# Performance work log

Measured on AMD Instinct MI355X. Metric: run time of the kernel, lower is better.

The kernel has to match this reference:

```python
import jax, jax.numpy as jnp
import numpy as np

N_NODES = 50000
N_GRAPHS = 64
NEG_SLOPE = 0.2


def gat_conv(x, src, dst, W, a_src, a_dst, b, n_nodes, concat):
    """PyG-style GATConv (eval mode, self-loops already in src/dst).
    x: [N, Fin], W: [Fin, H*C], a_src/a_dst: [H, C], b: [H*C] or [C].
    """
    H, C = a_src.shape
    h = (x @ W).reshape(n_nodes, H, C)                      # [N,H,C]
    al_src = jnp.einsum('nhc,hc->nh', h, a_src)             # [N,H]
    al_dst = jnp.einsum('nhc,hc->nh', h, a_dst)             # [N,H]
    e = jax.nn.leaky_relu(al_src[src] + al_dst[dst], NEG_SLOPE)  # [E,H]
    # softmax over incoming edges per destination node
    m = jax.ops.segment_max(e, dst, num_segments=n_nodes)   # [N,H]
    ex = jnp.exp(e - m[dst])
    s = jax.ops.segment_sum(ex, dst, num_segments=n_nodes)  # [N,H]
    alpha = ex / (s[dst] + 1e-16)                           # [E,H]
    # attention-weighted aggregation of source features
    out = jax.ops.segment_sum(h[src] * alpha[..., None], dst, num_segments=n_nodes)  # [N,H,C]
    out = out.reshape(n_nodes, H * C) if concat else out.mean(axis=1)
    return out + b


def setup_inputs() -> dict:
    key = jax.random.key(0)
    ks = jax.random.split(key, 12)
    n, e = N_NODES, 800000
    x = jax.random.normal(ks[0], (n, 500), dtype=jnp.float32)
    edge_index = jax.random.randint(ks[1], (2, e), 0, n, dtype=jnp.int64)
    batch = jnp.sort(jax.random.randint(ks[2], (n,), 0, N_GRAPHS, dtype=jnp.int64))
    hid, heads = 64, 4
    sc = 0.1
    W1 = jax.random.normal(ks[3], (500, heads * hid), dtype=jnp.float32) * sc
    a_src1 = jax.random.normal(ks[4], (heads, hid), dtype=jnp.float32) * sc
    a_dst1 = jax.random.normal(ks[5], (heads, hid), dtype=jnp.float32) * sc
    b1 = jnp.zeros((heads * hid,), dtype=jnp.float32)
    W2 = jax.random.normal(ks[6], (heads * hid, hid), dtype=jnp.float32) * sc
    a_src2 = jax.random.normal(ks[7], (1, hid), dtype=jnp.float32) * sc
    a_dst2 = jax.random.normal(ks[8], (1, hid), dtype=jnp.float32) * sc
    b2 = jnp.zeros((hid,), dtype=jnp.float32)
    Wl = jax.random.normal(ks[9], (hid, 2), dtype=jnp.float32) * sc
    bl = jnp.zeros((2,), dtype=jnp.float32)
    return dict(x=x, edge_index=edge_index, batch=batch,
                W1=W1, a_src1=a_src1, a_dst1=a_dst1, b1=b1,
                W2=W2, a_src2=a_src2, a_dst2=a_dst2, b2=b2,
                Wl=Wl, bl=bl)


def reference(x, edge_index, batch, W1, a_src1, a_dst1, b1,
              W2, a_src2, a_dst2, b2, Wl, bl):
    n = x.shape[0]
    # PyG GATConv adds self-loops by default
    loops = jnp.arange(n, dtype=edge_index.dtype)
    src = jnp.concatenate([edge_index[0], loops])
    dst = jnp.concatenate([edge_index[1], loops])
    h = jax.nn.relu(gat_conv(x, src, dst, W1, a_src1, a_dst1, b1, n, concat=True))
    h = jax.nn.relu(gat_conv(h, src, dst, W2, a_src2, a_dst2, b2, n, concat=False))
    # global mean pool over graphs
    sums = jax.ops.segment_sum(h, batch, num_segments=N_GRAPHS)      # [G, hid]
    cnt = jax.ops.segment_sum(jnp.ones((n,), h.dtype), batch, num_segments=N_GRAPHS)
    pooled = sums / jnp.maximum(cnt, 1.0)[:, None]
    return pooled @ Wl + bl                                          # [G, 2]
```

## Files before the change

kernel.cpp:

```cpp
#include <hip/hip_runtime.h>
#include <math.h>

#define NN   50000
#define NE   800000
#define NET  850000
#define NG   64
#define KIN  500
#define NEG  0.2f

typedef unsigned short ushort_t;
typedef __attribute__((ext_vector_type(8))) short bf8_t;
typedef __attribute__((ext_vector_type(8))) unsigned short us8_t;
typedef __attribute__((ext_vector_type(4))) float f4_t;

__device__ __forceinline__ float bf2f(ushort_t u) {
    unsigned v = ((unsigned)u) << 16;
    return __builtin_bit_cast(float, v);
}
__device__ __forceinline__ ushort_t f2bf(float f) {
    unsigned b = __builtin_bit_cast(unsigned, f);
    unsigned r = (b + 0x7FFFu + ((b >> 16) & 1u)) >> 16;
    return (ushort_t)r;
}

#define GLOAD_LDS(g, l)                                                        \
    __builtin_amdgcn_global_load_lds(                                          \
        (const __attribute__((address_space(1))) unsigned int*)(g),            \
        (__attribute__((address_space(3))) unsigned int*)(l), 16, 0, 0)

__global__ void k_deg(const int* __restrict__ ei, int* __restrict__ deg) {
    int e = blockIdx.x * 256 + threadIdx.x;
    if (e >= NET) return;
    int dst = (e < NE) ? ei[NE + e] : (e - NE);
    atomicAdd(&deg[dst], 1);
}

__global__ void k_scan_part(const int* __restrict__ deg, int* __restrict__ part) {
    __shared__ int s[256];
    int t = threadIdx.x;
    int i = blockIdx.x * 256 + t;
    s[t] = (i < NN) ? deg[i] : 0;
    __syncthreads();
    for (int off = 128; off > 0; off >>= 1) {
        if (t < off) s[t] += s[t + off];
        __syncthreads();
    }
    if (t == 0) part[blockIdx.x] = s[0];
}

__global__ void k_scan_top(int* __restrict__ part, int nb) {
    __shared__ int s[256];
    int t = threadIdx.x;
    int v = (t < nb) ? part[t] : 0;
    s[t] = v;
    __syncthreads();
    for (int off = 1; off < 256; off <<= 1) {
        int a = (t >= off) ? s[t - off] : 0;
        __syncthreads();
        s[t] += a;
        __syncthreads();
    }
    if (t < nb) part[t] = s[t] - v;
}

__global__ void k_scan_apply(const int* __restrict__ deg, const int* __restrict__ part,
                             int* __restrict__ rowptr) {
    __shared__ int s[256];
    int t = threadIdx.x;
    int i = blockIdx.x * 256 + t;
    int v = (i < NN) ? deg[i] : 0;
    s[t] = v;
    __syncthreads();
    for (int off = 1; off < 256; off <<= 1) {
        int a = (t >= off) ? s[t - off] : 0;
        __syncthreads();
        s[t] += a;
        __syncthreads();
    }
    if (i < NN) rowptr[i] = part[blockIdx.x] + s[t] - v;
    if (i == 0) rowptr[NN] = NET;
}

__global__ void k_fill(const int* __restrict__ ei, const int* __restrict__ rowptr,
                       int* __restrict__ cursor, int* __restrict__ csr) {
    int e = blockIdx.x * 256 + threadIdx.x;
    if (e >= NET) return;
    int src, dst;
    if (e < NE) { src = ei[e]; dst = ei[NE + e]; }
    else        { src = dst = e - NE; }
    int pos = atomicAdd(&cursor[dst], 1);
    csr[rowptr[dst] + pos] = src;
}

__global__ void k_cast_x(const float* __restrict__ x, ushort_t* __restrict__ xb) {
    int idx = blockIdx.x * 256 + threadIdx.x;
    if (idx >= 50048 * 128) return;
    int row = idx >> 7, k4 = (idx & 127) * 4;
    ushort4 o = make_ushort4(0, 0, 0, 0);
    if (row < NN && k4 < KIN) {
        float4 v = *(const float4*)&x[(size_t)row * KIN + k4];
        o.x = f2bf(v.x); o.y = f2bf(v.y); o.z = f2bf(v.z); o.w = f2bf(v.w);
    }
    *(ushort4*)&xb[(size_t)idx * 4] = o;
}

template <int KSRC, int KPAD, int NOUT>
__global__ void k_cast_wt(const float* __restrict__ W, ushort_t* __restrict__ Wt) {
    int idx = blockIdx.x * 256 + threadIdx.x;
    if (idx >= NOUT * KPAD) return;
    int n = idx / KPAD, k = idx - n * KPAD;
    float v = (k < KSRC) ? W[(size_t)k * NOUT + n] : 0.f;
    Wt[idx] = f2bf(v);
}

template <int K, int LDA, int BM, int BN, int WM, int FOUT, int HEADS>
__global__ __launch_bounds__(256) void k_mfma(
    const ushort_t* __restrict__ A, const ushort_t* __restrict__ Wt,
    const float* __restrict__ a_s, const float* __restrict__ a_d,
    ushort_t* __restrict__ Hb, float* __restrict__ als, float* __restrict__ ald)
{
    __shared__ __align__(16) ushort_t lA[BM * 32];
    __shared__ __align__(16) ushort_t lB[BN * 32];
    const int t    = threadIdx.x;
    const int row0 = blockIdx.y * BM;
    const int n0   = blockIdx.x * BN;
    const int ww   = t >> 6, lane = t & 63;
    const int wm   = ww % WM, wn = ww / WM;
    const int lrow = lane & 15, lq = lane >> 4;

    f4_t acc[4][4] = {};

    for (int k0 = 0; k0 < K; k0 += 32) {
#pragma unroll
        for (int i = 0; i < BM / 64; i++) {
            int c = i * 256 + t;
            int row = c >> 2, kq = c & 3;
            const ushort_t* gp = A + (size_t)(row0 + row) * LDA + k0 + kq * 8;
            GLOAD_LDS(gp, &lA[c * 8]);
        }
#pragma unroll
        for (int i = 0; i < BN / 64; i++) {
            int c = i * 256 + t;
            int row = c >> 2, kq = c & 3;
            const ushort_t* gp = Wt + (size_t)(n0 + row) * K + k0 + kq * 8;
            GLOAD_LDS(gp, &lB[c * 8]);
        }
        __syncthreads();
        bf8_t af[4], bfr[4];
#pragma unroll
        for (int i = 0; i < 4; i++)
            af[i] = *(const bf8_t*)&lA[(wm * 64 + i * 16 + lrow) * 32 + lq * 8];
#pragma unroll
        for (int j = 0; j < 4; j++)
            bfr[j] = *(const bf8_t*)&lB[(wn * 64 + j * 16 + lrow) * 32 + lq * 8];
#pragma unroll
        for (int i = 0; i < 4; i++)
#pragma unroll
            for (int j = 0; j < 4; j++)
                acc[i][j] = __builtin_amdgcn_mfma_f32_16x16x32_bf16(af[i], bfr[j], acc[i][j], 0, 0, 0);
        __syncthreads();
    }

    const int head = (n0 + wn * 64) >> 6;
    float as4[4], ad4[4];
#pragma unroll
    for (int j = 0; j < 4; j++) {
        as4[j] = a_s[head * 64 + j * 16 + lrow];
        ad4[j] = a_d[head * 64 + j * 16 + lrow];
    }
#pragma unroll
    for (int i = 0; i < 4; i++) {
#pragma unroll
        for (int r = 0; r < 4; r++) {
            int row = row0 + wm * 64 + i * 16 + lq * 4 + r;
            float v0 = acc[i][0][r], v1 = acc[i][1][r], v2 = acc[i][2][r], v3 = acc[i][3][r];
            if (row < NN) {
                size_t base = (size_t)row * FOUT + n0 + wn * 64 + lrow;
                Hb[base +  0] = f2bf(v0);
                Hb[base + 16] = f2bf(v1);
                Hb[base + 32] = f2bf(v2);
                Hb[base + 48] = f2bf(v3);
            }
            float ps = v0 * as4[0] + v1 * as4[1] + v2 * as4[2] + v3 * as4[3];
            float pd = v0 * ad4[0] + v1 * ad4[1] + v2 * ad4[2] + v3 * ad4[3];
#pragma unroll
            for (int off = 1; off < 16; off <<= 1) {
                ps += __shfl_xor(ps, off);
                pd += __shfl_xor(pd, off);
            }
            if (lrow == 0 && row < NN) {
                als[(size_t)row * HEADS + head] = ps;
                ald[(size_t)row * HEADS + head] = pd;
            }
        }
    }
}

#define CAP1 128
__global__ __launch_bounds__(256) void k_agg1(
    const int* __restrict__ rowptr, const int* __restrict__ csr,
    const ushort_t* __restrict__ Hb, const float* __restrict__ als,
    const float* __restrict__ ald, const float* __restrict__ bias,
    ushort_t* __restrict__ OutB)
{
    __shared__ float salpha[4][CAP1 * 4];
    int w = threadIdx.x >> 6, lane = threadIdx.x & 63;
    int dst = blockIdx.x * 4 + w;
    if (dst >= NN) return;
    float* Aw = salpha[w];
    const int beg = rowptr[dst], end = rowptr[dst + 1];
    const int deg = end - beg;

    const int hd   = lane & 3;
    const int slot = lane >> 2;
    const float adst = ald[dst * 4 + hd];
    float m = -1e30f, s = 0.f;
    for (int k = slot; k < deg; k += 16) {
        int src = csr[beg + k];
        float e = als[src * 4 + hd] + adst;
        e = (e > 0.f) ? e : NEG * e;
        if (k < CAP1) Aw[k * 4 + hd] = e;
        float mn = fmaxf(m, e);
        s = s * __expf(m - mn) + __expf(e - mn);
        m = mn;
    }
#pragma unroll
    for (int off = 4; off < 64; off <<= 1) {
        float mo = __shfl_xor(m, off);
        float so = __shfl_xor(s, off);
        float mn = fmaxf(m, mo);
        s = s * __expf(m - mn) + so * __expf(mo - mn);
        m = mn;
    }
    float inv = 1.f / (s + 1e-16f);
    int cap4 = (deg < CAP1 ? deg : CAP1) * 4;
    for (int j = lane; j < cap4; j += 64)
        Aw[j] = __expf(Aw[j] - m) * inv;

    const int slot2 = lane >> 5;
    const int head2 = (lane >> 3) & 3;
    const int f0    = (lane & 7) * 8;
    const float m2  = __shfl(m, head2);
    const float i2  = __shfl(inv, head2);
    const float ad2 = __shfl(adst, head2);

    float facc[8] = {};
    int  k0    = 0;
    int  ke    = slot2;
    bool valid = ke < deg;
    int  src   = csr[beg + (valid ? ke : 0)];
    us8_t xv   = *(const us8_t*)&Hb[(size_t)src * 256 + head2 * 64 + f0];
    while (true) {
        int k0n = k0 + 2;
        bool more = k0n < deg;
        int src2 = 0; us8_t xv2 = {}; bool valid2 = false;
        if (more) {
            int ke2 = k0n + slot2;
            valid2 = ke2 < deg;
            src2 = csr[beg + (valid2 ? ke2 : 0)];
            xv2  = *(const us8_t*)&Hb[(size_t)src2 * 256 + head2 * 64 + f0];
        }
        float al;
        if (ke < CAP1) {
            al = Aw[ke * 4 + head2];
        } else {
            float e = als[src * 4 + head2] + ad2;
            e = (e > 0.f) ? e : NEG * e;
            al = __expf(e - m2) * i2;
        }
        if (!valid) al = 0.f;
#pragma unroll
        for (int j = 0; j < 8; j++)
            facc[j] += al * bf2f((ushort_t)xv[j]);
        if (!more) break;
        k0 = k0n; ke = k0 + slot2; valid = valid2; src = src2; xv = xv2;
    }
#pragma unroll
    for (int j = 0; j < 8; j++) facc[j] += __shfl_xor(facc[j], 32);
    if (lane < 32) {
        us8_t o8;
#pragma unroll
        for (int j = 0; j < 8; j++) {
            float o = facc[j] + bias[head2 * 64 + f0 + j];
            o = (o > 0.f) ? o : 0.f;
            o8[j] = f2bf(o);
        }
        *(us8_t*)&OutB[(size_t)dst * 256 + head2 * 64 + f0] = o8;
    }
}

#define CAP2 128
__global__ __launch_bounds__(256) void k_agg2(
    const int* __restrict__ rowptr, const int* __restrict__ csr,
    const ushort_t* __restrict__ Hb, const float* __restrict__ als,
    const float* __restrict__ ald, const float* __restrict__ bias,
    float* __restrict__ OutF)
{
    __shared__ float salpha2[4][CAP2];
    int w = threadIdx.x >> 6, lane = threadIdx.x & 63;
    int dst = blockIdx.x * 4 + w;
    if (dst >= NN) return;
    float* Aw = salpha2[w];
    const int beg = rowptr[dst], end = rowptr[dst + 1];
    const int deg = end - beg;
    const float adst = ald[dst];

    float m = -1e30f, s = 0.f;
    for (int k = lane; k < deg; k += 64) {
        int src = csr[beg + k];
        float e = als[src] + adst;
        e = (e > 0.f) ? e : NEG * e;
        if (k < CAP2) Aw[k] = e;
        float mn = fmaxf(m, e);
        s = s * __expf(m - mn) + __expf(e - mn);
        m = mn;
    }
#pragma unroll
    for (int off = 1; off < 64; off <<= 1) {
        float mo = __shfl_xor(m, off);
        float so = __shfl_xor(s, off);
        float mn = fmaxf(m, mo);
        s = s * __expf(m - mn) + so * __expf(mo - mn);
        m = mn;
    }
    float inv = 1.f / (s + 1e-16f);
    int cap = deg < CAP2 ? deg : CAP2;
    for (int j = lane; j < cap; j += 64)
        Aw[j] = __expf(Aw[j] - m) * inv;

    const int slot2 = lane >> 4;
    const int f0    = (lane & 15) * 4;
    float facc[4] = {};
    int  k0    = 0;
    int  ke    = slot2;
    bool valid = ke < deg;
    int  src   = csr[beg + (valid ? ke : 0)];
    ushort4 xv = *(const ushort4*)&Hb[(size_t)src * 64 + f0];
    while (true) {
        int k0n = k0 + 4;
        bool more = k0n < deg;
        int src2 = 0; ushort4 xv2 = make_ushort4(0, 0, 0, 0); bool valid2 = false;
        if (more) {
            int ke2 = k0n + slot2;
            valid2 = ke2 < deg;
            src2 = csr[beg + (valid2 ? ke2 : 0)];
            xv2  = *(const ushort4*)&Hb[(size_t)src2 * 64 + f0];
        }
        float al;
        if (ke < CAP2) al = Aw[ke];
        else {
            float e = als[src] + adst;
            e = (e > 0.f) ? e : NEG * e;
            al = __expf(e - m) * inv;
        }
        if (!valid) al = 0.f;
        facc[0] += al * bf2f(xv.x);
        facc[1] += al * bf2f(xv.y);
        facc[2] += al * bf2f(xv.z);
        facc[3] += al * bf2f(xv.w);
        if (!more) break;
        k0 = k0n; ke = k0 + slot2; valid = valid2; src = src2; xv = xv2;
    }
#pragma unroll
    for (int j = 0; j < 4; j++) {
        facc[j] += __shfl_xor(facc[j], 16);
        facc[j] += __shfl_xor(facc[j], 32);
    }
    if (lane < 16) {
        float4 o;
        float* op = &o.x;
#pragma unroll
        for (int j = 0; j < 4; j++) {
            float v = facc[j] + bias[f0 + j];
            op[j] = (v > 0.f) ? v : 0.f;
        }
        *(float4*)&OutF[(size_t)dst * 64 + f0] = o;
    }
}

__global__ void k_pool_final(const float* __restrict__ out2, const int* __restrict__ batch,
                             const float* __restrict__ Wl, const float* __restrict__ bl,
                             float* __restrict__ out)
{
    int g = blockIdx.x;
    int lo, hi;
    { int a = 0, b = NN; while (a < b) { int mm = (a + b) >> 1; if (batch[mm] < g) a = mm + 1; else b = mm; } lo = a; }
    { int a = lo, b = NN; while (a < b) { int mm = (a + b) >> 1; if (batch[mm] < g + 1) a = mm + 1; else b = mm; } hi = a; }
    int t = threadIdx.x, c = t & 63, r = t >> 6;
    float s = 0.f;
    for (int n = lo + r; n < hi; n += 4) s += out2[(size_t)n * 64 + c];
    __shared__ float red[256];
    red[t] = s;
    __syncthreads();
    if (t < 64) {
        float p = red[t] + red[t + 64] + red[t + 128] + red[t + 192];
        int cntv = hi - lo;
        p /= (float)(cntv > 0 ? cntv : 1);
        float r0 = p * Wl[t * 2 + 0];
        float r1 = p * Wl[t * 2 + 1];
#pragma unroll
        for (int off = 32; off > 0; off >>= 1) {
            r0 += __shfl_xor(r0, off);
            r1 += __shfl_xor(r1, off);
        }
        if (t == 0) {
            out[g * 2 + 0] = r0 + bl[0];
            out[g * 2 + 1] = r1 + bl[1];
        }
    }
}

extern "C" void kernel_launch(void* const* d_in, const int* in_sizes, int n_in,
                              void* d_out, int out_size, void* d_ws, size_t ws_size,
                              hipStream_t stream)
{
    const float* x    = (const float*)d_in[0];
    const int*   ei   = (const int*)  d_in[1];
    const int*   batch= (const int*)  d_in[2];
    const float* W1   = (const float*)d_in[3];
    const float* as1  = (const float*)d_in[4];
    const float* ad1  = (const float*)d_in[5];
    const float* b1   = (const float*)d_in[6];
    const float* W2   = (const float*)d_in[7];
    const float* as2  = (const float*)d_in[8];
    const float* ad2  = (const float*)d_in[9];
    const float* b2   = (const float*)d_in[10];
    const float* Wl   = (const float*)d_in[11];
    const float* bl   = (const float*)d_in[12];
    float* out = (float*)d_out;

    int*   deg    = (int*)d_ws;
    int*   cursor = deg + 50048;
    int*   part   = cursor + 50048;
    int*   rowptr = part + 256;
    int*   csr    = rowptr + 50064;
    ushort_t* xb  = (ushort_t*)(csr + 850048);
    ushort_t* Wt1 = xb + (size_t)50048 * 512;
    ushort_t* Wt2 = Wt1 + 131072;
    ushort_t* h1b = Wt2 + 16384;
    float* al1s   = (float*)(h1b + (size_t)50000 * 256);
    float* al1d   = al1s + 200000;
    float* al2s   = al1d + 200000;
    float* al2d   = al2s + 50000;
    ushort_t* out1b = xb;
    ushort_t* h2b   = xb + 13000000;
    float*    out2  = (float*)(xb + 16400000);

    hipMemsetAsync(deg, 0, 2 * 50048 * sizeof(int), stream);

    k_deg       <<<(NET + 255) / 256, 256, 0, stream>>>(ei, deg);
    k_scan_part <<<196, 256, 0, stream>>>(deg, part);
    k_scan_top  <<<1,   256, 0, stream>>>(part, 196);
    k_scan_apply<<<196, 256, 0, stream>>>(deg, part, rowptr);
    k_fill      <<<(NET + 255) / 256, 256, 0, stream>>>(ei, rowptr, cursor, csr);

    k_cast_x<<<(50048 * 128 + 255) / 256, 256, 0, stream>>>(x, xb);
    k_cast_wt<500, 512, 256><<<(256 * 512 + 255) / 256, 256, 0, stream>>>(W1, Wt1);
    k_cast_wt<256, 256, 64> <<<(64 * 256 + 255) / 256, 256, 0, stream>>>(W2, Wt2);

    k_mfma<512, 512, 128, 128, 2, 256, 4><<<dim3(2, 391), 256, 0, stream>>>(
        xb, Wt1, as1, ad1, h1b, al1s, al1d);
    k_agg1<<<(NN + 3) / 4, 256, 0, stream>>>(rowptr, csr, h1b, al1s, al1d, b1, out1b);
    hipMemsetAsync(out1b + (size_t)50000 * 256, 0, (size_t)176 * 256 * sizeof(ushort_t), stream);

    k_mfma<256, 256, 256, 64, 4, 64, 1><<<dim3(1, 196), 256, 0, stream>>>(
        out1b, Wt2, as2, ad2, h2b, al2s, al2d);
    k_agg2<<<(NN + 3) / 4, 256, 0, stream>>>(rowptr, csr, h2b, al2s, al2d, b2, out2);

    k_pool_final<<<NG, 256, 0, stream>>>(out2, batch, Wl, bl, out);
}
```

Before: 500.2 us.

## Store projected node features as FP8 to halve gather traffic in aggregation

The GEMM epilogues now write the projected features h1/h2 as FP8 (e4m3) bytes instead of bf16. Both aggregation kernels are remapped to gather 16 bytes or 8 bytes per lane of FP8 data, processing more edges per iteration, and decode with the hardware FP8 convert. The first source gather is also issued before the softmax pass to overlap its latency. This targets the memory-bound random gathers in aggregation, at the cost of a large precision loss in the features, which may exceed the tolerance.

```diff
diff --git a/kernel.cpp b/kernel.cpp
--- a/kernel.cpp
+++ b/kernel.cpp
@@ -12,6 +12,8 @@
 typedef __attribute__((ext_vector_type(8))) short bf8_t;
 typedef __attribute__((ext_vector_type(8))) unsigned short us8_t;
 typedef __attribute__((ext_vector_type(4))) float f4_t;
+typedef __attribute__((ext_vector_type(4))) unsigned u4_t;
+typedef __attribute__((ext_vector_type(2))) unsigned u2_t;
 
 __device__ __forceinline__ float bf2f(ushort_t u) {
     unsigned v = ((unsigned)u) << 16;
@@ -22,6 +24,41 @@
     unsigned r = (b + 0x7FFFu + ((b >> 16) & 1u)) >> 16;
     return (ushort_t)r;
 }
+
+#if __has_builtin(__builtin_amdgcn_cvt_f32_fp8)
+#define FP8DEC(w, b) __builtin_amdgcn_cvt_f32_fp8((w), (b))
+#else
+__device__ __forceinline__ float fp8_sw_dec(unsigned w, int b) {
+    unsigned by = (w >> (8 * b)) & 0xFFu;
+    unsigned s = by >> 7, e = (by >> 3) & 15u, m = by & 7u;
+    float v = e ? __builtin_bit_cast(float, ((e + 120u) << 23) | (m << 20))
+                : (float)m * 0.001953125f;
+    return s ? -v : v;
+}
+#define FP8DEC(w, b) fp8_sw_dec((w), (b))
+#endif
+
+#if __has_builtin(__builtin_amdgcn_cvt_pk_fp8_f32)
+__device__ __forceinline__ unsigned char f2fp8(float f) {
+    return (unsigned char)(__builtin_amdgcn_cvt_pk_fp8_f32(f, 0.f, 0u, false) & 0xFFu);
+}
+#else
+__device__ __forceinline__ unsigned char f2fp8(float f) {
+    unsigned u = __builtin_bit_cast(unsigned, f);
+    unsigned sgn = (u >> 24) & 0x80u;
+    float a = fabsf(f);
+    if (!(a < 448.f)) return (unsigned char)(sgn | 0x7Eu);
+    if (a < 0.015625f) {
+        int m = (int)(a * 512.f + 0.5f);
+        return (unsigned char)(sgn | (m > 7 ? 8 : m));
+    }
+    unsigned r = u + 0x7FFFFu + ((u >> 20) & 1u);
+    unsigned e = (r >> 23) & 0xFFu;
+    unsigned m = (r >> 20) & 7u;
+    if (e > 135u) return (unsigned char)(sgn | 0x7Eu);
+    return (unsigned char)(sgn | ((e - 120u) << 3) | m);
+}
+#endif
 
 #define GLOAD_LDS(g, l)                                                        \
     __builtin_amdgcn_global_load_lds(                                          \
@@ -117,7 +154,7 @@
 __global__ __launch_bounds__(256) void k_mfma(
     const ushort_t* __restrict__ A, const ushort_t* __restrict__ Wt,
     const float* __restrict__ a_s, const float* __restrict__ a_d,
-    ushort_t* __restrict__ Hb, float* __restrict__ als, float* __restrict__ ald)
+    unsigned char* __restrict__ Hb, float* __restrict__ als, float* __restrict__ ald)
 {
     __shared__ __align__(16) ushort_t lA[BM * 32];
     __shared__ __align__(16) ushort_t lB[BN * 32];
@@ -176,10 +213,10 @@
             float v0 = acc[i][0][r], v1 = acc[i][1][r], v2 = acc[i][2][r], v3 = acc[i][3][r];
             if (row < NN) {
                 size_t base = (size_t)row * FOUT + n0 + wn * 64 + lrow;
-                Hb[base +  0] = f2bf(v0);
-                Hb[base + 16] = f2bf(v1);
-                Hb[base + 32] = f2bf(v2);
-                Hb[base + 48] = f2bf(v3);
+                Hb[base +  0] = f2fp8(v0);
+                Hb[base + 16] = f2fp8(v1);
+                Hb[base + 32] = f2fp8(v2);
+                Hb[base + 48] = f2fp8(v3);
             }
             float ps = v0 * as4[0] + v1 * as4[1] + v2 * as4[2] + v3 * as4[3];
             float pd = v0 * ad4[0] + v1 * ad4[1] + v2 * ad4[2] + v3 * ad4[3];
@@ -199,7 +236,7 @@
 #define CAP1 128
 __global__ __launch_bounds__(256) void k_agg1(
     const int* __restrict__ rowptr, const int* __restrict__ csr,
-    const ushort_t* __restrict__ Hb, const float* __restrict__ als,
+    const unsigned char* __restrict__ Hb, const float* __restrict__ als,
     const float* __restrict__ ald, const float* __restrict__ bias,
     ushort_t* __restrict__ OutB)
 {
@@ -211,13 +248,22 @@
     const int beg = rowptr[dst], end = rowptr[dst + 1];
     const int deg = end - beg;
 
-    const int hd   = lane & 3;
-    const int slot = lane >> 2;
+    const int hd    = lane & 3;
+    const int slot  = lane >> 2;
+    const int slot2 = lane >> 4;
+    const int head2 = (lane >> 2) & 3;
+    const int f0    = (lane & 3) * 16;
+
+    int  ke    = slot2;
+    bool valid = ke < deg;
+    int  src   = csr[beg + (valid ? ke : 0)];
+    u4_t xv    = *(const u4_t*)&Hb[(size_t)src * 256 + head2 * 64 + f0];
+
     const float adst = ald[dst * 4 + hd];
     float m = -1e30f, s = 0.f;
     for (int k = slot; k < deg; k += 16) {
-        int src = csr[beg + k];
-        float e = als[src * 4 + hd] + adst;
+        int sk = csr[beg + k];
+        float e = als[sk * 4 + hd] + adst;
         e = (e > 0.f) ? e : NEG * e;
         if (k < CAP1) Aw[k * 4 + hd] = e;
         float mn = fmaxf(m, e);
@@ -237,62 +283,66 @@
     for (int j = lane; j < cap4; j += 64)
         Aw[j] = __expf(Aw[j] - m) * inv;
 
-    const int slot2 = lane >> 5;
-    const int head2 = (lane >> 3) & 3;
-    const int f0    = (lane & 7) * 8;
     const float m2  = __shfl(m, head2);
     const float i2  = __shfl(inv, head2);
     const float ad2 = __shfl(adst, head2);
 
-    float facc[8] = {};
-    int  k0    = 0;
-    int  ke    = slot2;
-    bool valid = ke < deg;
-    int  src   = csr[beg + (valid ? ke : 0)];
-    us8_t xv   = *(const us8_t*)&Hb[(size_t)src * 256 + head2 * 64 + f0];
+    float facc[16] = {};
+    int k0 = 0;
     while (true) {
-        int k0n = k0 + 2;
+        int k0n = k0 + 4;
         bool more = k0n < deg;
-        int src2 = 0; us8_t xv2 = {}; bool valid2 = false;
+        int srcn = 0; u4_t xvn = {}; bool validn = false;
         if (more) {
-            int ke2 = k0n + slot2;
-            valid2 = ke2 < deg;
-            src2 = csr[beg + (valid2 ? ke2 : 0)];
-            xv2  = *(const us8_t*)&Hb[(size_t)src2 * 256 + head2 * 64 + f0];
-        }
-        float al;
-        if (ke < CAP1) {
-            al = Aw[ke * 4 + head2];
-        } else {
-            float e = als[src * 4 + head2] + ad2;
-            e = (e > 0.f) ? e : NEG * e;
-            al = __expf(e - m2) * i2;
-        }
-        if (!valid) al = 0.f;
-#pragma unroll
-        for (int j = 0; j < 8; j++)
-            facc[j] += al * bf2f((ushort_t)xv[j]);
+            int ken = k0n + slot2;
+            validn = ken < deg;
+            srcn = csr[beg + (validn ? ken : 0)];
+            xvn  = *(const u4_t*)&Hb[(size_t)srcn * 256 + head2 * 64 + f0];
+        }
+        float al = 0.f;
+        if (valid) {
+            if (ke < CAP1) {
+                al = Aw[ke * 4 + head2];
+            } else {
+                float e = als[src * 4 + head2] + ad2;
+                e = (e > 0.f) ? e : NEG * e;
+                al = __expf(e - m2) * i2;
+            }
+        }
+#pragma unroll
+        for (int wd = 0; wd < 4; wd++) {
+            unsigned wv = xv[wd];
+            facc[wd * 4 + 0] += al * FP8DEC(wv, 0);
+            facc[wd * 4 + 1] += al * FP8DEC(wv, 1);
+            facc[wd * 4 + 2] += al * FP8DEC(wv, 2);
+            facc[wd * 4 + 3] += al * FP8DEC(wv, 3);
+        }
         if (!more) break;
-        k0 = k0n; ke = k0 + slot2; valid = valid2; src = src2; xv = xv2;
-    }
-#pragma unroll
-    for (int j = 0; j < 8; j++) facc[j] += __shfl_xor(facc[j], 32);
-    if (lane < 32) {
-        us8_t o8;
+        k0 = k0n; ke = k0 + slot2; valid = validn; src = srcn; xv = xvn;
+    }
+#pragma unroll
+    for (int j = 0; j < 16; j++) {
+        facc[j] += __shfl_xor(facc[j], 16);
+        facc[j] += __shfl_xor(facc[j], 32);
+    }
+    if (lane < 16) {
+        us8_t oa, ob;
 #pragma unroll
         for (int j = 0; j < 8; j++) {
-            float o = facc[j] + bias[head2 * 64 + f0 + j];
-            o = (o > 0.f) ? o : 0.f;
-            o8[j] = f2bf(o);
-        }
-        *(us8_t*)&OutB[(size_t)dst * 256 + head2 * 64 + f0] = o8;
+            float o  = facc[j]     + bias[head2 * 64 + f0 + j];
+            float o2 = facc[8 + j] + bias[head2 * 64 + f0 + 8 + j];
+            oa[j] = f2bf(o  > 0.f ? o  : 0.f);
+            ob[j] = f2bf(o2 > 0.f ? o2 : 0.f);
+        }
+        *(us8_t*)&OutB[(size_t)dst * 256 + head2 * 64 + f0]     = oa;
+        *(us8_t*)&OutB[(size_t)dst * 256 + head2 * 64 + f0 + 8] = ob;
     }
 }
 
 #define CAP2 128
 __global__ __launch_bounds__(256) void k_agg2(
     const int* __restrict__ rowptr, const int* __restrict__ csr,
-    const ushort_t* __restrict__ Hb, const float* __restrict__ als,
+    const unsigned char* __restrict__ Hb, const float* __restrict__ als,
     const float* __restrict__ ald, const float* __restrict__ bias,
     float* __restrict__ OutF)
 {
@@ -305,10 +355,18 @@
     const int deg = end - beg;
     const float adst = ald[dst];
 
+    const int slot2 = lane >> 3;
+    const int f0    = (lane & 7) * 8;
+
+    int  ke    = slot2;
+    bool valid = ke < deg;
+    int  src   = csr[beg + (valid ? ke : 0)];
+    u2_t xv    = *(const u2_t*)&Hb[(size_t)src * 64 + f0];
+
     float m = -1e30f, s = 0.f;
     for (int k = lane; k < deg; k += 64) {
-        int src = csr[beg + k];
-        float e = als[src] + adst;
+        int sk = csr[beg + k];
+        float e = als[sk] + adst;
         e = (e > 0.f) ? e : NEG * e;
         if (k < CAP2) Aw[k] = e;
         float mn = fmaxf(m, e);
@@ -328,53 +386,57 @@
     for (int j = lane; j < cap; j += 64)
         Aw[j] = __expf(Aw[j] - m) * inv;
 
-    const int slot2 = lane >> 4;
-    const int f0    = (lane & 15) * 4;
-    float facc[4] = {};
-    int  k0    = 0;
-    int  ke    = slot2;
-    bool valid = ke < deg;
-    int  src   = csr[beg + (valid ? ke : 0)];
-    ushort4 xv = *(const ushort4*)&Hb[(size_t)src * 64 + f0];
+    float facc[8] = {};
+    int k0 = 0;
     while (true) {
-        int k0n = k0 + 4;
+        int k0n = k0 + 8;
         bool more = k0n < deg;
-        int src2 = 0; ushort4 xv2 = make_ushort4(0, 0, 0, 0); bool valid2 = false;
+        int srcn = 0; u2_t xvn = {}; bool validn = false;
         if (more) {
-            int ke2 = k0n + slot2;
-            valid2 = ke2 < deg;
-            src2 = csr[beg + (valid2 ? ke2 : 0)];
-            xv2  = *(const ushort4*)&Hb[(size_t)src2 * 64 + f0];
-        }
-        float al;
-        if (ke < CAP2) al = Aw[ke];
-        else {
-            float e = als[src] + adst;
-            e = (e > 0.f) ? e : NEG * e;
-            al = __expf(e - m) * inv;
-        }
-        if (!valid) al = 0.f;
-        facc[0] += al * bf2f(xv.x);
-        facc[1] += al * bf2f(xv.y);
-        facc[2] += al * bf2f(xv.z);
-        facc[3] += al * bf2f(xv.w);
+            int ken = k0n + slot2;
+            validn = ken < deg;
+            srcn = csr[beg + (validn ? ken : 0)];
+            xvn  = *(const u2_t*)&Hb[(size_t)srcn * 64 + f0];
+        }
+        float al = 0.f;
+        if (valid) {
+            if (ke < CAP2) {
+                al = Aw[ke];
+            } else {
+                float e = als[src] + adst;
+                e = (e > 0.f) ? e : NEG * e;
+                al = __expf(e - m) * inv;
+            }
+        }
+#pragma unroll
+        for (int wd = 0; wd < 2; wd++) {
+            unsigned wv = xv[wd];
+            facc[wd * 4 + 0] += al * FP8DEC(wv, 0);
+            facc[wd * 4 + 1] += al * FP8DEC(wv, 1);
+            facc[wd * 4 + 2] += al * FP8DEC(wv, 2);
+            facc[wd * 4 + 3] += al * FP8DEC(wv, 3);
+        }
         if (!more) break;
-        k0 = k0n; ke = k0 + slot2; valid = valid2; src = src2; xv = xv2;
-    }
-#pragma unroll
-    for (int j = 0; j < 4; j++) {
+        k0 = k0n; ke = k0 + slot2; valid = validn; src = srcn; xv = xvn;
+    }
+#pragma unroll
+    for (int j = 0; j < 8; j++) {
+        facc[j] += __shfl_xor(facc[j], 8);
         facc[j] += __shfl_xor(facc[j], 16);
         facc[j] += __shfl_xor(facc[j], 32);
     }
-    if (lane < 16) {
-        float4 o;
-        float* op = &o.x;
+    if (lane < 8) {
+        float4 oa, ob;
+        float* pa = &oa.x; float* pb = &ob.x;
 #pragma unroll
         for (int j = 0; j < 4; j++) {
-            float v = facc[j] + bias[f0 + j];
-            op[j] = (v > 0.f) ? v : 0.f;
-        }
-        *(float4*)&OutF[(size_t)dst * 64 + f0] = o;
+            float v  = facc[j]     + bias[f0 + j];
+            float v2 = facc[4 + j] + bias[f0 + 4 + j];
+            pa[j] = (v  > 0.f) ? v  : 0.f;
+            pb[j] = (v2 > 0.f) ? v2 : 0.f;
+        }
+        *(float4*)&OutF[(size_t)dst * 64 + f0]     = oa;
+        *(float4*)&OutF[(size_t)dst * 64 + f0 + 4] = ob;
     }
 }
 
@@ -438,12 +500,13 @@
     ushort_t* Wt1 = xb + (size_t)50048 * 512;
     ushort_t* Wt2 = Wt1 + 131072;
     ushort_t* h1b = Wt2 + 16384;
+    unsigned char* h1b8 = (unsigned char*)h1b;
     float* al1s   = (float*)(h1b + (size_t)50000 * 256);
     float* al1d   = al1s + 200000;
     float* al2s   = al1d + 200000;
     float* al2d   = al2s + 50000;
     ushort_t* out1b = xb;
-    ushort_t* h2b   = xb + 13000000;
+    unsigned char* h2b8 = (unsigned char*)(xb + 13000000);
     float*    out2  = (float*)(xb + 16400000);
 
     hipMemsetAsync(deg, 0, 2 * 50048 * sizeof(int), stream);
@@ -459,13 +522,13 @@
     k_cast_wt<256, 256, 64> <<<(64 * 256 + 255) / 256, 256, 0, stream>>>(W2, Wt2);
 
     k_mfma<512, 512, 128, 128, 2, 256, 4><<<dim3(2, 391), 256, 0, stream>>>(
-        xb, Wt1, as1, ad1, h1b, al1s, al1d);
-    k_agg1<<<(NN + 3) / 4, 256, 0, stream>>>(rowptr, csr, h1b, al1s, al1d, b1, out1b);
+        xb, Wt1, as1, ad1, h1b8, al1s, al1d);
+    k_agg1<<<(NN + 3) / 4, 256, 0, stream>>>(rowptr, csr, h1b8, al1s, al1d, b1, out1b);
     hipMemsetAsync(out1b + (size_t)50000 * 256, 0, (size_t)176 * 256 * sizeof(ushort_t), stream);
 
     k_mfma<256, 256, 256, 64, 4, 64, 1><<<dim3(1, 196), 256, 0, stream>>>(
-        out1b, Wt2, as2, ad2, h2b, al2s, al2d);
-    k_agg2<<<(NN + 3) / 4, 256, 0, stream>>>(rowptr, csr, h2b, al2s, al2d, b2, out2);
+        out1b, Wt2, as2, ad2, h2b8, al2s, al2d);
+    k_agg2<<<(NN + 3) / 4, 256, 0, stream>>>(rowptr, csr, h2b8, al2s, al2d, b2, out2);
 
     k_pool_final<<<NG, 256, 0, stream>>>(out2, batch, Wl, bl, out);
 }
```

Result: faster. 463.8 us (-7.3%).
